# Kernel optimization log

Hardware: AMD Instinct MI355X
Metric: run time of the kernel (lower is better)

The kernel has to match this reference:

```python
import jax, jax.numpy as jnp
import numpy as np

FP8_E4M3_MAX = 448.0
FP4_E2M1_MAX = 6.0
BLOCK = 16  # NVFP4 block-scale granularity


def _round_e4m3(x):
    """Round non-negative values to fp8 e4m3 grid (3 mantissa bits, min normal 2^-6, max 448)."""
    a = jnp.abs(x)
    e = jnp.clip(jnp.floor(jnp.log2(jnp.where(a > 0, a, 1.0))), -6.0, 8.0)
    s = jnp.exp2(e)
    q = jnp.round(a / s * 8.0) / 8.0 * s
    q = jnp.clip(q, 0.0, FP8_E4M3_MAX)
    return jnp.where(a > 0, q, 0.0)


def _round_e2m1(x):
    """Round to fp4 e2m1 grid: +/- {0, 0.5, 1, 1.5, 2, 3, 4, 6}."""
    sgn = jnp.sign(x)
    a = jnp.clip(jnp.abs(x), 0.0, FP4_E2M1_MAX)
    e = jnp.clip(jnp.floor(jnp.log2(jnp.where(a > 0, a, 1.0))), 0.0, 2.0)
    step = jnp.exp2(e) * 0.5  # 0.5 in [0,2), 1 in [2,4), 2 in [4,6]
    q = jnp.round(a / step) * step
    return sgn * jnp.clip(q, 0.0, FP4_E2M1_MAX)


def quant_nvfp4(t):
    """Dynamic NVFP4 quantization (vLLM scaled_fp4_quant semantics).
    Returns (q_fp4 [R, K/16, 16], block_scale_e4m3 [R, K/16], global_scale []).
    Dequant: q * block_scale / global_scale."""
    gs = (FP8_E4M3_MAX * FP4_E2M1_MAX) / jnp.max(jnp.abs(t))
    tb = t.reshape(t.shape[0], -1, BLOCK)
    block_amax = jnp.max(jnp.abs(tb), axis=-1)              # [R, K/16]
    bs = _round_e4m3(block_amax / FP4_E2M1_MAX * gs)         # e4m3 block scales
    safe_bs = jnp.where(bs > 0, bs, 1.0)
    q = _round_e2m1(tb * (gs / safe_bs)[..., None])
    q = jnp.where((bs > 0)[..., None], q, 0.0)
    return q, bs, gs


def setup_inputs() -> dict:
    key = jax.random.key(0)
    kx, kw = jax.random.split(key)
    tokens, hidden = 8192, 4096
    x = jax.random.normal(kx, (tokens, 2 * hidden), dtype=jnp.float32)
    w = jax.random.uniform(kw, (hidden, hidden), dtype=jnp.float32)
    return {"x": x, "w": w}


def reference(x, w):
    d = x.shape[-1] // 2
    # SiluAndMul
    y = jax.nn.silu(x[..., :d]) * x[..., d:]                # [T, H]
    # dynamic NVFP4 quant of activation and weight
    qy, sy, gy = quant_nvfp4(y)
    qw, sw, gw = quant_nvfp4(w)
    # cutlass_scaled_fp4_mm: out = (qy*sy) @ (qw*sw)^T * alpha, alpha = 1/(gy*gw)
    a = (qy * sy[..., None]).reshape(y.shape)               # [T, H]
    b = (qw * sw[..., None]).reshape(w.shape)               # [H, H]
    alpha = 1.0 / (gy * gw)
    return (a @ b.T) * alpha
```

## Files before the change

kernel.cpp:

```cpp
#include <hip/hip_runtime.h>
#include <hip/hip_bf16.h>

typedef __attribute__((ext_vector_type(8))) short bf16x8;
typedef __attribute__((ext_vector_type(4))) float f32x4;


__device__ __forceinline__ float silu_mul_f(float a, float b) {
  float s = 1.0f / (1.0f + expf(-a));
  return (a * s) * b;
}

__device__ __forceinline__ int flog2(float a) {
  return (int)((__float_as_uint(a) >> 23) & 255u) - 127;
}
__device__ __forceinline__ float exp2i(int e) {
  return __uint_as_float((unsigned)(e + 127) << 23);
}

__device__ __forceinline__ float round_e4m3_f(float a) {
  if (!(a > 0.0f)) return 0.0f;
  int e = flog2(a);
  e = e < -6 ? -6 : (e > 8 ? 8 : e);
  float q = rintf(a * exp2i(3 - e)) * exp2i(e - 3);
  return fminf(q, 448.0f);
}

__device__ __forceinline__ float round_e2m1_f(float x) {
  float a = fminf(fabsf(x), 6.0f);
  if (!(a > 0.0f)) return 0.0f;
  int e = flog2(a);
  e = e < 0 ? 0 : (e > 2 ? 2 : e);
  float q = rintf(a * exp2i(1 - e)) * exp2i(e - 1);
  q = fminf(q, 6.0f);
  return (x < 0.0f) ? -q : q;
}

__global__ void init_scal_kernel(float* scal) {
  if (threadIdx.x < 2) scal[threadIdx.x] = 0.0f;
}


__global__ void fused_amax_kernel(const float* __restrict__ x, const float* __restrict__ w,
                                  float* __restrict__ scal, int tokens, int hidden) {
  float m = 0.0f;
  if ((int)blockIdx.x < tokens) {
    const float* x1 = x + (size_t)blockIdx.x * (size_t)(2 * hidden);
    const float* x2 = x1 + hidden;
    int n4 = hidden >> 2;
    for (int c = threadIdx.x; c < n4; c += blockDim.x) {
      float4 v1 = ((const float4*)x1)[c];
      float4 v2 = ((const float4*)x2)[c];
      m = fmaxf(m, fabsf(silu_mul_f(v1.x, v2.x)));
      m = fmaxf(m, fabsf(silu_mul_f(v1.y, v2.y)));
      m = fmaxf(m, fabsf(silu_mul_f(v1.z, v2.z)));
      m = fmaxf(m, fabsf(silu_mul_f(v1.w, v2.w)));
    }
  } else {
    const float* row = w + (size_t)(blockIdx.x - tokens) * (size_t)hidden;
    int n4 = hidden >> 2;
    for (int c = threadIdx.x; c < n4; c += blockDim.x) {
      float4 v = ((const float4*)row)[c];
      m = fmaxf(m, fmaxf(fmaxf(fabsf(v.x), fabsf(v.y)), fmaxf(fabsf(v.z), fabsf(v.w))));
    }
  }
#pragma unroll
  for (int off = 32; off > 0; off >>= 1) m = fmaxf(m, __shfl_xor(m, off));
  __shared__ float sm[4];
  if ((threadIdx.x & 63) == 0) sm[threadIdx.x >> 6] = m;
  __syncthreads();
  if (threadIdx.x == 0) {
    float mm = fmaxf(fmaxf(sm[0], sm[1]), fmaxf(sm[2], sm[3]));
    unsigned int* dst = (unsigned int*)(scal + ((int)blockIdx.x < tokens ? 0 : 1));
    atomicMax(dst, __float_as_uint(mm));
  }
}


__device__ __forceinline__ void quant_block16(const float* y, float gs, __hip_bfloat16* dst) {
  float bamax = 0.0f;
#pragma unroll
  for (int k = 0; k < 16; ++k) bamax = fmaxf(bamax, fabsf(y[k]));
  float bs = round_e4m3_f(bamax * (1.0f / 6.0f) * 6.0f == 0.0f ? 0.0f : bamax / 6.0f * gs);
  float r = gs / (bs > 0.0f ? bs : 1.0f);
  union { bf16x8 v[2]; unsigned short h[16]; } u;
#pragma unroll
  for (int k = 0; k < 16; ++k) {
    float q = round_e2m1_f(y[k] * r);
    float val = q * bs;
    u.h[k] = (unsigned short)(__float_as_uint(val) >> 16);
  }
  ((bf16x8*)dst)[0] = u.v[0];
  ((bf16x8*)dst)[1] = u.v[1];
}

__global__ void fused_quant_kernel(const float* __restrict__ x, const float* __restrict__ w,
                                   __hip_bfloat16* __restrict__ A, __hip_bfloat16* __restrict__ B,
                                   const float* __restrict__ scal, int tokens, int hidden) {
  int nb = hidden >> 4;
  if ((int)blockIdx.x < tokens) {
    const float gs = 2688.0f / scal[0];
    int row = blockIdx.x;
    const float* x1 = x + (size_t)row * (size_t)(2 * hidden);
    const float* x2 = x1 + hidden;
    for (int b = threadIdx.x; b < nb; b += blockDim.x) {
      const float* p1 = x1 + b * 16;
      const float* p2 = x2 + b * 16;
      float y[16];
#pragma unroll
      for (int j = 0; j < 4; ++j) {
        float4 v1 = *(const float4*)(p1 + 4 * j);
        float4 v2 = *(const float4*)(p2 + 4 * j);
        y[4 * j + 0] = silu_mul_f(v1.x, v2.x);
        y[4 * j + 1] = silu_mul_f(v1.y, v2.y);
        y[4 * j + 2] = silu_mul_f(v1.z, v2.z);
        y[4 * j + 3] = silu_mul_f(v1.w, v2.w);
      }
      quant_block16(y, gs, A + (size_t)row * (size_t)hidden + (size_t)b * 16);
    }
  } else {
    const float gs = 2688.0f / scal[1];
    int row = blockIdx.x - tokens;
    const float* src = w + (size_t)row * (size_t)hidden;
    for (int b = threadIdx.x; b < nb; b += blockDim.x) {
      const float* p = src + b * 16;
      float y[16];
#pragma unroll
      for (int j = 0; j < 4; ++j) {
        float4 v = *(const float4*)(p + 4 * j);
        y[4 * j + 0] = v.x; y[4 * j + 1] = v.y; y[4 * j + 2] = v.z; y[4 * j + 3] = v.w;
      }
      quant_block16(y, gs, B + (size_t)row * (size_t)hidden + (size_t)b * 16);
    }
  }
}


__device__ __forceinline__ void gload_lds16(const void* g, void* l) {
  __builtin_amdgcn_global_load_lds(
      (const __attribute__((address_space(1))) void*)(uintptr_t)g,
      (__attribute__((address_space(3))) void*)(uintptr_t)l, 16, 0, 0);
}

template <unsigned IMM>
__device__ __forceinline__ bf16x8 lds_read16o(unsigned addr) {
  bf16x8 r;
  asm volatile("ds_read_b128 %0, %1 offset:%c2" : "=&v"(r) : "v"(addr), "i"(IMM));
  return r;
}

__device__ __forceinline__ f32x4 mfma_(bf16x8 a, bf16x8 b, f32x4 c) {
  return __builtin_amdgcn_mfma_f32_16x16x32_bf16(a, b, c, 0, 0, 0);
}

#define SP1 __builtin_amdgcn_s_setprio(1)
#define SP0 __builtin_amdgcn_s_setprio(0)
#define SCHEDB __builtin_amdgcn_sched_barrier(0)
#define WAITL(n) do { asm volatile("s_waitcnt lgkmcnt(" #n ")" ::: "memory"); SCHEDB; } while (0)
#define VMW4 do { asm volatile("s_waitcnt vmcnt(4)" ::: "memory"); } while (0)

#define STAGEA(PP, HH, KSB) do {                                        \
    const char* _s = pa + (KSB) + (HH) * 64;                            \
    gload_lds16(_s, ldsStA + (PP) * 32768 + (HH) * 16384);              \
    gload_lds16(_s + rowBig, ldsStA + (PP) * 32768 + (HH) * 16384 + 8192); } while (0)

#define STAGEB(PP, HH, KSB) do {                                        \
    const char* _s = pb + (KSB) + (HH) * 64;                            \
    gload_lds16(_s, ldsStB + (PP) * 32768 + (HH) * 16384);              \
    gload_lds16(_s + rowBig, ldsStB + (PP) * 32768 + (HH) * 16384 + 8192); } while (0)

#define RDA4(DST, PP, HH, MB) do {                                              \
    DST[0] = lds_read16o<(PP)*32768u + (HH)*16384u + ((MB)+0)*1024u>(vA);       \
    DST[1] = lds_read16o<(PP)*32768u + (HH)*16384u + ((MB)+1)*1024u>(vA);       \
    DST[2] = lds_read16o<(PP)*32768u + (HH)*16384u + ((MB)+2)*1024u>(vA);       \
    DST[3] = lds_read16o<(PP)*32768u + (HH)*16384u + ((MB)+3)*1024u>(vA); } while (0)

#define RDB4(DST, PP, HH) do {                                                  \
    DST[0] = lds_read16o<(PP)*32768u + (HH)*16384u + 0u>(vB);                   \
    DST[1] = lds_read16o<(PP)*32768u + (HH)*16384u + 1024u>(vB);                \
    DST[2] = lds_read16o<(PP)*32768u + (HH)*16384u + 2048u>(vB);                \
    DST[3] = lds_read16o<(PP)*32768u + (HH)*16384u + 3072u>(vB); } while (0)

#define MFMA16(AF, BF, MB) do {                                                  \
    acc[(MB)+0][0] = mfma_(AF[0], BF[0], acc[(MB)+0][0]);                        \
    acc[(MB)+1][0] = mfma_(AF[1], BF[0], acc[(MB)+1][0]);                        \
    acc[(MB)+2][0] = mfma_(AF[2], BF[0], acc[(MB)+2][0]);                        \
    acc[(MB)+3][0] = mfma_(AF[3], BF[0], acc[(MB)+3][0]);                        \
    acc[(MB)+0][1] = mfma_(AF[0], BF[1], acc[(MB)+0][1]);                        \
    acc[(MB)+1][1] = mfma_(AF[1], BF[1], acc[(MB)+1][1]);                        \
    acc[(MB)+2][1] = mfma_(AF[2], BF[1], acc[(MB)+2][1]);                        \
    acc[(MB)+3][1] = mfma_(AF[3], BF[1], acc[(MB)+3][1]);                        \
    acc[(MB)+0][2] = mfma_(AF[0], BF[2], acc[(MB)+0][2]);                        \
    acc[(MB)+1][2] = mfma_(AF[1], BF[2], acc[(MB)+1][2]);                        \
    acc[(MB)+2][2] = mfma_(AF[2], BF[2], acc[(MB)+2][2]);                        \
    acc[(MB)+3][2] = mfma_(AF[3], BF[2], acc[(MB)+3][2]);                        \
    acc[(MB)+0][3] = mfma_(AF[0], BF[3], acc[(MB)+0][3]);                        \
    acc[(MB)+1][3] = mfma_(AF[1], BF[3], acc[(MB)+1][3]);                        \
    acc[(MB)+2][3] = mfma_(AF[2], BF[3], acc[(MB)+2][3]);                        \
    acc[(MB)+3][3] = mfma_(AF[3], BF[3], acc[(MB)+3][3]); } while (0)

#define TILE(P, KSB) do {                                                        \
                                                              \
    STAGEA((P)^1, 0, KSB);                                                       \
    RDA4(aY, P, 0, 4);                                                           \
    WAITL(4);                                                                    \
    SP1; MFMA16(aX, bb0, 0); SP0;                                                \
                                                              \
    STAGEB((P)^1, 0, KSB);                                                       \
    VMW4;                                                                        \
    __builtin_amdgcn_s_barrier(); SCHEDB;                                        \
    RDA4(aX, P, 1, 0); RDB4(bb1, P, 1);                                          \
    WAITL(8);                                                                    \
    SP1; MFMA16(aY, bb0, 4); SP0;                                                \
                                                              \
    STAGEA((P)^1, 1, KSB);                                                       \
    RDA4(aY, P, 1, 4);                                                           \
    WAITL(4);                                                                    \
    SP1; MFMA16(aX, bb1, 0); SP0;                                                \
                                                              \
    STAGEB((P)^1, 1, KSB);                                                       \
    WAITL(0);                                                                    \
    VMW4;                                                                        \
    __builtin_amdgcn_s_barrier(); SCHEDB;                                        \
    RDA4(aX, (P)^1, 0, 0); RDB4(bb0, (P)^1, 0); SCHEDB;                          \
    SP1; MFMA16(aY, bb1, 4); SP0;                                                \
  } while (0)

__global__ __launch_bounds__(512, 2) void gemm_bt_kernel(
    const __hip_bfloat16* __restrict__ A, const __hip_bfloat16* __restrict__ B,
    float* __restrict__ C, const float* __restrict__ scal, int M, int N, int K) {
  __shared__ __align__(16) char lds[131072];

  const int nbm = M >> 8, nbn = N >> 8;
  int wg = blockIdx.x, bm, bn;
  if ((nbm & 7) == 0) {
    int band = nbm >> 3;
    int x = wg & 7, c = wg >> 3;
    bm = x * band + (c % band);
    bn = c / band;
  } else {
    bm = wg / nbn; bn = wg % nbn;
  }
  const int brow = bm << 8, bcol = bn << 8;

  const int tid = threadIdx.x;
  const int lane = tid & 63;
  const int wave = tid >> 6;
  const int wm = wave >> 2, wn = wave & 3;

  const int srow = tid >> 2;
  const int slc = (tid & 3) ^ ((tid >> 3) & 3);
  const char* pa = (const char*)(A + (size_t)(brow + srow) * K + slc * 8);
  const char* pb = (const char*)(B + (size_t)(bcol + srow) * K + slc * 8);
  const size_t rowBig = (size_t)128 * K * 2;
  char* ldsStA = lds + tid * 16;
  char* ldsStB = lds + 65536 + tid * 16;

  const unsigned ldsBase = (unsigned)(uintptr_t)lds;
  const unsigned xoff = (unsigned)((lane & 15) * 64) +
                        ((((unsigned)(lane >> 4)) ^ (((unsigned)lane >> 1) & 3u)) << 4);
  const unsigned vA = ldsBase + (unsigned)(wm * 8192) + xoff;
  const unsigned vB = ldsBase + 65536u + (unsigned)(wn * 4096) + xoff;

  f32x4 acc[8][4] = {};
  bf16x8 aX[4], aY[4], bb0[4], bb1[4];

  STAGEA(0, 0, 0); STAGEB(0, 0, 0); STAGEA(0, 1, 0); STAGEB(0, 1, 0);
  asm volatile("s_waitcnt vmcnt(0)" ::: "memory");
  __syncthreads();
  RDA4(aX, 0, 0, 0); RDB4(bb0, 0, 0); SCHEDB;

  const int nt = K >> 6;
  for (int it = 0; it < (nt >> 1); ++it) {
    int t0 = it << 1;
    int ks0 = (t0 + 1) * 128;
    int ks1 = (t0 + 2 == nt) ? 0 : (t0 + 2) * 128;
    TILE(0, ks0);
    TILE(1, ks1);
  }
  asm volatile("s_waitcnt lgkmcnt(0)" ::: "memory");
  asm volatile("s_waitcnt vmcnt(0)" ::: "memory");

  float gy = 2688.0f / scal[0];
  float gw = 2688.0f / scal[1];
  float alpha = 1.0f / (gy * gw);

#pragma unroll
  for (int m = 0; m < 8; ++m) {
    int rbase = brow + wm * 128 + m * 16 + ((lane >> 4) << 2);
#pragma unroll
    for (int n = 0; n < 4; ++n) {
      int col = bcol + wn * 64 + n * 16 + (lane & 15);
#pragma unroll
      for (int rg = 0; rg < 4; ++rg) {
        C[(size_t)(rbase + rg) * N + col] = acc[m][n][rg] * alpha;
      }
    }
  }
}


extern "C" void kernel_launch(void* const* d_in, const int* in_sizes, int n_in,
                              void* d_out, int out_size, void* d_ws, size_t ws_size,
                              hipStream_t stream) {
  const float* x = (const float*)d_in[0];
  const float* w = (const float*)d_in[1];
  float* out = (float*)d_out;

  int hidden = 1;
  while ((long long)hidden * hidden < (long long)in_sizes[1]) hidden <<= 1;
  int tokens = in_sizes[0] / (2 * hidden);

  char* ws = (char*)d_ws;
  __hip_bfloat16* Aq = (__hip_bfloat16*)ws;
  __hip_bfloat16* Bq = (__hip_bfloat16*)(ws + (size_t)tokens * hidden * 2);
  float* scal = (float*)(ws + (size_t)tokens * hidden * 2 + (size_t)hidden * hidden * 2);

  init_scal_kernel<<<1, 64, 0, stream>>>(scal);
  fused_amax_kernel<<<tokens + hidden, 256, 0, stream>>>(x, w, scal, tokens, hidden);
  fused_quant_kernel<<<tokens + hidden, 256, 0, stream>>>(x, w, Aq, Bq, scal, tokens, hidden);

  int grid = (tokens >> 8) * (hidden >> 8);
  gemm_bt_kernel<<<grid, 512, 0, stream>>>(Aq, Bq, out, scal, tokens, hidden, hidden);
}
```

Baseline: 453.6 us.

## Rewrite amax and quant as grid-stride kernels with float4-per-thread coalescing

Replaces the per-row amax and quant kernels with grid-stride kernels on a fixed 2048-block grid, where each thread handles one float4. In the quant kernel the 16-element block amax is now formed from four adjacent lanes with two xor shuffles, so each warp's loads and bf16 stores become fully contiguous. Before, each thread read 64 contiguous bytes at a 64-byte stride across lanes. The aim is better memory coalescing and fewer, longer-lived blocks in the bandwidth-bound pre-GEMM passes. The amax kernel also tracks activation and weight maxima in every block, which means two atomics per block.

```diff
diff --git a/kernel.cpp b/kernel.cpp
--- a/kernel.cpp
+++ b/kernel.cpp
@@ -40,97 +40,87 @@
 }
 
 
-__global__ void fused_amax_kernel(const float* __restrict__ x, const float* __restrict__ w,
-                                  float* __restrict__ scal, int tokens, int hidden) {
-  float m = 0.0f;
-  if ((int)blockIdx.x < tokens) {
-    const float* x1 = x + (size_t)blockIdx.x * (size_t)(2 * hidden);
-    const float* x2 = x1 + hidden;
-    int n4 = hidden >> 2;
-    for (int c = threadIdx.x; c < n4; c += blockDim.x) {
-      float4 v1 = ((const float4*)x1)[c];
-      float4 v2 = ((const float4*)x2)[c];
-      m = fmaxf(m, fabsf(silu_mul_f(v1.x, v2.x)));
-      m = fmaxf(m, fabsf(silu_mul_f(v1.y, v2.y)));
-      m = fmaxf(m, fabsf(silu_mul_f(v1.z, v2.z)));
-      m = fmaxf(m, fabsf(silu_mul_f(v1.w, v2.w)));
+__global__ void amax2_kernel(const float* __restrict__ x, const float* __restrict__ w,
+                             float* __restrict__ scal, long actU, long wU,
+                             int hidden, int hqLog) {
+  float mA = 0.0f, mW = 0.0f;
+  const long stride = (long)gridDim.x * blockDim.x;
+  const long hqm = (1L << hqLog) - 1;
+  const long total = actU + wU;
+  for (long u = (long)blockIdx.x * blockDim.x + threadIdx.x; u < total; u += stride) {
+    if (u < actU) {
+      long row = u >> hqLog;
+      long c = u & hqm;
+      const float* xr = x + ((row * (long)hidden) << 1);
+      float4 v1 = ((const float4*)xr)[c];
+      float4 v2 = ((const float4*)(xr + hidden))[c];
+      mA = fmaxf(mA, fabsf(silu_mul_f(v1.x, v2.x)));
+      mA = fmaxf(mA, fabsf(silu_mul_f(v1.y, v2.y)));
+      mA = fmaxf(mA, fabsf(silu_mul_f(v1.z, v2.z)));
+      mA = fmaxf(mA, fabsf(silu_mul_f(v1.w, v2.w)));
+    } else {
+      float4 v = ((const float4*)w)[u - actU];
+      mW = fmaxf(mW, fmaxf(fmaxf(fabsf(v.x), fabsf(v.y)), fmaxf(fabsf(v.z), fabsf(v.w))));
     }
-  } else {
-    const float* row = w + (size_t)(blockIdx.x - tokens) * (size_t)hidden;
-    int n4 = hidden >> 2;
-    for (int c = threadIdx.x; c < n4; c += blockDim.x) {
-      float4 v = ((const float4*)row)[c];
-      m = fmaxf(m, fmaxf(fmaxf(fabsf(v.x), fabsf(v.y)), fmaxf(fabsf(v.z), fabsf(v.w))));
-    }
   }
 #pragma unroll
-  for (int off = 32; off > 0; off >>= 1) m = fmaxf(m, __shfl_xor(m, off));
-  __shared__ float sm[4];
-  if ((threadIdx.x & 63) == 0) sm[threadIdx.x >> 6] = m;
+  for (int off = 32; off > 0; off >>= 1) {
+    mA = fmaxf(mA, __shfl_xor(mA, off));
+    mW = fmaxf(mW, __shfl_xor(mW, off));
+  }
+  __shared__ float sA[4], sW[4];
+  if ((threadIdx.x & 63) == 0) { sA[threadIdx.x >> 6] = mA; sW[threadIdx.x >> 6] = mW; }
   __syncthreads();
   if (threadIdx.x == 0) {
-    float mm = fmaxf(fmaxf(sm[0], sm[1]), fmaxf(sm[2], sm[3]));
-    unsigned int* dst = (unsigned int*)(scal + ((int)blockIdx.x < tokens ? 0 : 1));
-    atomicMax(dst, __float_as_uint(mm));
-  }
-}
-
-
-__device__ __forceinline__ void quant_block16(const float* y, float gs, __hip_bfloat16* dst) {
-  float bamax = 0.0f;
-#pragma unroll
-  for (int k = 0; k < 16; ++k) bamax = fmaxf(bamax, fabsf(y[k]));
-  float bs = round_e4m3_f(bamax * (1.0f / 6.0f) * 6.0f == 0.0f ? 0.0f : bamax / 6.0f * gs);
-  float r = gs / (bs > 0.0f ? bs : 1.0f);
-  union { bf16x8 v[2]; unsigned short h[16]; } u;
-#pragma unroll
-  for (int k = 0; k < 16; ++k) {
-    float q = round_e2m1_f(y[k] * r);
-    float val = q * bs;
-    u.h[k] = (unsigned short)(__float_as_uint(val) >> 16);
-  }
-  ((bf16x8*)dst)[0] = u.v[0];
-  ((bf16x8*)dst)[1] = u.v[1];
-}
-
-__global__ void fused_quant_kernel(const float* __restrict__ x, const float* __restrict__ w,
-                                   __hip_bfloat16* __restrict__ A, __hip_bfloat16* __restrict__ B,
-                                   const float* __restrict__ scal, int tokens, int hidden) {
-  int nb = hidden >> 4;
-  if ((int)blockIdx.x < tokens) {
-    const float gs = 2688.0f / scal[0];
-    int row = blockIdx.x;
-    const float* x1 = x + (size_t)row * (size_t)(2 * hidden);
-    const float* x2 = x1 + hidden;
-    for (int b = threadIdx.x; b < nb; b += blockDim.x) {
-      const float* p1 = x1 + b * 16;
-      const float* p2 = x2 + b * 16;
-      float y[16];
-#pragma unroll
-      for (int j = 0; j < 4; ++j) {
-        float4 v1 = *(const float4*)(p1 + 4 * j);
-        float4 v2 = *(const float4*)(p2 + 4 * j);
-        y[4 * j + 0] = silu_mul_f(v1.x, v2.x);
-        y[4 * j + 1] = silu_mul_f(v1.y, v2.y);
-        y[4 * j + 2] = silu_mul_f(v1.z, v2.z);
-        y[4 * j + 3] = silu_mul_f(v1.w, v2.w);
-      }
-      quant_block16(y, gs, A + (size_t)row * (size_t)hidden + (size_t)b * 16);
+    atomicMax((unsigned int*)(scal + 0),
+              __float_as_uint(fmaxf(fmaxf(sA[0], sA[1]), fmaxf(sA[2], sA[3]))));
+    atomicMax((unsigned int*)(scal + 1),
+              __float_as_uint(fmaxf(fmaxf(sW[0], sW[1]), fmaxf(sW[2], sW[3]))));
+  }
+}
+
+
+__global__ void quant2_kernel(const float* __restrict__ x, const float* __restrict__ w,
+                              __hip_bfloat16* __restrict__ A, __hip_bfloat16* __restrict__ B,
+                              const float* __restrict__ scal, long actU, long wU,
+                              int hidden, int hqLog) {
+  const float gsA = 2688.0f / scal[0];
+  const float gsW = 2688.0f / scal[1];
+  const long stride = (long)gridDim.x * blockDim.x;
+  const long hqm = (1L << hqLog) - 1;
+  const long total = actU + wU;
+  for (long u = (long)blockIdx.x * blockDim.x + threadIdx.x; u < total; u += stride) {
+    float y0, y1, y2, y3, gs;
+    unsigned short* dst;
+    if (u < actU) {
+      long row = u >> hqLog;
+      long c = u & hqm;
+      const float* xr = x + ((row * (long)hidden) << 1) + (c << 2);
+      float4 v1 = *(const float4*)xr;
+      float4 v2 = *(const float4*)(xr + hidden);
+      y0 = silu_mul_f(v1.x, v2.x);
+      y1 = silu_mul_f(v1.y, v2.y);
+      y2 = silu_mul_f(v1.z, v2.z);
+      y3 = silu_mul_f(v1.w, v2.w);
+      gs = gsA;
+      dst = (unsigned short*)A + (u << 2);
+    } else {
+      float4 v = ((const float4*)w)[u - actU];
+      y0 = v.x; y1 = v.y; y2 = v.z; y3 = v.w;
+      gs = gsW;
+      dst = (unsigned short*)B + ((u - actU) << 2);
     }
-  } else {
-    const float gs = 2688.0f / scal[1];
-    int row = blockIdx.x - tokens;
-    const float* src = w + (size_t)row * (size_t)hidden;
-    for (int b = threadIdx.x; b < nb; b += blockDim.x) {
-      const float* p = src + b * 16;
-      float y[16];
-#pragma unroll
-      for (int j = 0; j < 4; ++j) {
-        float4 v = *(const float4*)(p + 4 * j);
-        y[4 * j + 0] = v.x; y[4 * j + 1] = v.y; y[4 * j + 2] = v.z; y[4 * j + 3] = v.w;
-      }
-      quant_block16(y, gs, B + (size_t)row * (size_t)hidden + (size_t)b * 16);
-    }
+    float lm = fmaxf(fmaxf(fabsf(y0), fabsf(y1)), fmaxf(fabsf(y2), fabsf(y3)));
+    lm = fmaxf(lm, __shfl_xor(lm, 1));
+    lm = fmaxf(lm, __shfl_xor(lm, 2));
+    float bs = round_e4m3_f(lm / 6.0f * gs);
+    float r = gs / (bs > 0.0f ? bs : 1.0f);
+    ushort4 o;
+    o.x = (unsigned short)(__float_as_uint(round_e2m1_f(y0 * r) * bs) >> 16);
+    o.y = (unsigned short)(__float_as_uint(round_e2m1_f(y1 * r) * bs) >> 16);
+    o.z = (unsigned short)(__float_as_uint(round_e2m1_f(y2 * r) * bs) >> 16);
+    o.w = (unsigned short)(__float_as_uint(round_e2m1_f(y3 * r) * bs) >> 16);
+    *(ushort4*)dst = o;
   }
 }
 
@@ -199,24 +189,20 @@
     acc[(MB)+3][3] = mfma_(AF[3], BF[3], acc[(MB)+3][3]); } while (0)
 
 #define TILE(P, KSB) do {                                                        \
-                                                              \
     STAGEA((P)^1, 0, KSB);                                                       \
     RDA4(aY, P, 0, 4);                                                           \
     WAITL(4);                                                                    \
     SP1; MFMA16(aX, bb0, 0); SP0;                                                \
-                                                              \
     STAGEB((P)^1, 0, KSB);                                                       \
     VMW4;                                                                        \
     __builtin_amdgcn_s_barrier(); SCHEDB;                                        \
     RDA4(aX, P, 1, 0); RDB4(bb1, P, 1);                                          \
     WAITL(8);                                                                    \
     SP1; MFMA16(aY, bb0, 4); SP0;                                                \
-                                                              \
     STAGEA((P)^1, 1, KSB);                                                       \
     RDA4(aY, P, 1, 4);                                                           \
     WAITL(4);                                                                    \
     SP1; MFMA16(aX, bb1, 0); SP0;                                                \
-                                                              \
     STAGEB((P)^1, 1, KSB);                                                       \
     WAITL(0);                                                                    \
     VMW4;                                                                        \
@@ -234,8 +220,8 @@
   int wg = blockIdx.x, bm, bn;
   if ((nbm & 7) == 0) {
     int band = nbm >> 3;
-    int x = wg & 7, c = wg >> 3;
-    bm = x * band + (c % band);
+    int xcd = wg & 7, c = wg >> 3;
+    bm = xcd * band + (c % band);
     bn = c / band;
   } else {
     bm = wg / nbn; bn = wg % nbn;
@@ -315,9 +301,13 @@
   __hip_bfloat16* Bq = (__hip_bfloat16*)(ws + (size_t)tokens * hidden * 2);
   float* scal = (float*)(ws + (size_t)tokens * hidden * 2 + (size_t)hidden * hidden * 2);
 
+  long actU = (long)tokens * hidden / 4;
+  long wU = (long)hidden * hidden / 4;
+  int hqLog = __builtin_ctz((unsigned)(hidden >> 2));
+
   init_scal_kernel<<<1, 64, 0, stream>>>(scal);
-  fused_amax_kernel<<<tokens + hidden, 256, 0, stream>>>(x, w, scal, tokens, hidden);
-  fused_quant_kernel<<<tokens + hidden, 256, 0, stream>>>(x, w, Aq, Bq, scal, tokens, hidden);
+  amax2_kernel<<<2048, 256, 0, stream>>>(x, w, scal, actU, wU, hidden, hqLog);
+  quant2_kernel<<<2048, 256, 0, stream>>>(x, w, Aq, Bq, scal, actU, wU, hidden, hqLog);
 
   int grid = (tokens >> 8) * (hidden >> 8);
   gemm_bt_kernel<<<grid, 512, 0, stream>>>(Aq, Bq, out, scal, tokens, hidden, hidden);
```

After: 414.0 us. 1.1x faster.
